# Performance work log

Measured on AMD Instinct MI355X. Metric: run time of the kernel, lower is better.

The kernel has to match this reference:

```python
import jax, jax.numpy as jnp
import numpy as np

DIM = 512
HEADS = 8
HEAD_DIM = DIM // HEADS
SCALE = HEAD_DIM ** -0.5


def setup_inputs() -> dict:
    key = jax.random.key(0)
    k1, k2, k3, k4, k5 = jax.random.split(key, 5)
    x = jax.random.normal(k1, (2, 4096, DIM), dtype=jnp.float32)
    # qkv Linear: weight [3*dim, dim], bias [3*dim]; proj: [dim, dim], [dim]
    w_qkv = jax.random.normal(k2, (3 * DIM, DIM), dtype=jnp.float32) * (DIM ** -0.5)
    b_qkv = jax.random.normal(k3, (3 * DIM,), dtype=jnp.float32) * 0.02
    w_proj = jax.random.normal(k4, (DIM, DIM), dtype=jnp.float32) * (DIM ** -0.5)
    b_proj = jax.random.normal(k5, (DIM,), dtype=jnp.float32) * 0.02
    return {"x": x, "w_qkv": w_qkv, "b_qkv": b_qkv, "w_proj": w_proj, "b_proj": b_proj}


def reference(x, w_qkv, b_qkv, w_proj, b_proj):
    B, N, C = x.shape
    qkv = x @ w_qkv.T + b_qkv  # [B, N, 3C]
    qkv = qkv.reshape(B, N, 3, HEADS, HEAD_DIM).transpose(2, 0, 3, 1, 4)  # [3,B,H,N,hd]
    q, k, v = qkv[0], qkv[1], qkv[2]
    attn = jnp.einsum('bhnd,bhmd->bhnm', q, k) * SCALE  # explicit NxN matrix
    attn = jax.nn.softmax(attn, axis=-1)
    out = jnp.einsum('bhnm,bhmd->bhnd', attn, v)  # [B,H,N,hd]
    out = out.transpose(0, 2, 1, 3).reshape(B, N, C)
    return out @ w_proj.T + b_proj
```

## Files before the change

### kernel.cpp

```cpp
#include <hip/hip_runtime.h>

typedef __bf16 bf16x8 __attribute__((ext_vector_type(8)));
typedef __bf16 bf16x4 __attribute__((ext_vector_type(4)));
typedef __bf16 bf16x2 __attribute__((ext_vector_type(2)));
typedef float  floatx4 __attribute__((ext_vector_type(4)));
typedef unsigned int uint32;
typedef uint32 uintx4 __attribute__((ext_vector_type(4)));

#define MFMA16(a,b,c) __builtin_amdgcn_mfma_f32_16x16x32_bf16(a,b,c,0,0,0)

constexpr int DIM  = 512;
constexpr int SEQ  = 4096;
constexpr int HD   = 64;
constexpr float QSCALE = 0.1803368801111244f;

static __device__ inline __bf16 f2bf(float f) {
    unsigned int u = __builtin_bit_cast(unsigned int, f);
    u += 0x7fffu + ((u >> 16) & 1u);
    return __builtin_bit_cast(__bf16, (unsigned short)(u >> 16));
}
#if __has_builtin(__builtin_amdgcn_cvt_pk_bf16_f32)
static __device__ inline bf16x2 pk2(float a, float b) {
    return __builtin_amdgcn_cvt_pk_bf16_f32(a, b);
}
#else
static __device__ inline bf16x2 pk2(float a, float b) {
    bf16x2 r; r[0] = f2bf(a); r[1] = f2bf(b); return r;
}
#endif
#if __has_builtin(__builtin_amdgcn_exp2f)
#define EXP2(x) __builtin_amdgcn_exp2f(x)
#else
#define EXP2(x) exp2f(x)
#endif
static __device__ inline bf16x8 cvt8(floatx4 lo, floatx4 hi) {
    uintx4 w;
    w[0] = __builtin_bit_cast(uint32, pk2(lo[0], lo[1]));
    w[1] = __builtin_bit_cast(uint32, pk2(lo[2], lo[3]));
    w[2] = __builtin_bit_cast(uint32, pk2(hi[0], hi[1]));
    w[3] = __builtin_bit_cast(uint32, pk2(hi[2], hi[3]));
    return __builtin_bit_cast(bf16x8, w);
}

static __device__ inline void gload16(const __bf16* g, __bf16* l) {
#if __has_builtin(__builtin_amdgcn_global_load_lds)
    __builtin_amdgcn_global_load_lds(
        (const __attribute__((address_space(1))) unsigned int*)g,
        (__attribute__((address_space(3))) unsigned int*)l, 16, 0, 0);
#else
    *(bf16x8*)(l + (threadIdx.x & 63)*8) = *(const bf16x8*)g;
#endif
}


__global__ __launch_bounds__(256)
void cvt_bf16(const float* __restrict__ X, const float* __restrict__ Wq,
              const float* __restrict__ Wp,
              __bf16* __restrict__ Xb, __bf16* __restrict__ Wqb,
              __bf16* __restrict__ Wpb)
{
    const int slice = blockIdx.y;
    const float* src;
    __bf16* dst;
    int n8;
    if (slice == 0)      { src = X;  dst = Xb;  n8 = (2*SEQ*DIM)/8; }
    else if (slice == 1) { src = Wq; dst = Wqb; n8 = (3*DIM*DIM)/8; }
    else                 { src = Wp; dst = Wpb; n8 = (DIM*DIM)/8; }
    const int i = blockIdx.x * 256 + threadIdx.x;
    if (i >= n8) return;
    const floatx4 lo = *(const floatx4*)(src + (size_t)i*8);
    const floatx4 hi = *(const floatx4*)(src + (size_t)i*8 + 4);
    *(bf16x8*)(dst + (size_t)i*8) = cvt8(lo, hi);
}

__global__ __launch_bounds__(256)
void gemm_qkv(const __bf16* __restrict__ X, const __bf16* __restrict__ W,
              const float* __restrict__ bias,
              __bf16* __restrict__ Qb, __bf16* __restrict__ Kb, __bf16* __restrict__ Vb)
{
    __shared__ __bf16 As[2][128*32];
    __shared__ __bf16 Bs[2][128*32];
    const int tid  = threadIdx.x;
    const int lane = tid & 63;
    const int wave = tid >> 6;
    const int quad = lane >> 4;
    const int l16  = lane & 15;
    const int waveM = wave >> 1, waveN = wave & 1;
    const int mBase = blockIdx.x * 128;
    const int nBase = blockIdx.y * 128;
    const int which = nBase >> 9;

    floatx4 zero = {0.f, 0.f, 0.f, 0.f};
    floatx4 acc[4][4];
    for (int i = 0; i < 4; i++)
        for (int j = 0; j < 4; j++) acc[i][j] = zero;

    const int lrow = lane >> 2;
    const int lcol = (lane & 3) * 8;

    const __bf16* ga = X + (size_t)(mBase + wave*16 + lrow)*DIM + lcol;
    const __bf16* gb = W + (size_t)(nBase + wave*16 + lrow)*DIM + lcol;

    auto STAGE = [&](int it, int b) {
        const int k0 = it * 32;
        gload16(ga + k0,            &As[b][(wave*16)*32]);
        gload16(ga + 64*DIM + k0,   &As[b][(64 + wave*16)*32]);
        gload16(gb + k0,            &Bs[b][(wave*16)*32]);
        gload16(gb + 64*DIM + k0,   &Bs[b][(64 + wave*16)*32]);
    };

    STAGE(0, 0);
    __syncthreads();

    for (int it = 0; it < 16; ++it) {
        const int cur = it & 1;
        if (it < 15) STAGE(it + 1, cur ^ 1);

        bf16x8 af[4], bfr[4];
        for (int mi = 0; mi < 4; mi++)
            af[mi]  = *(const bf16x8*)&As[cur][(waveM*64 + mi*16 + l16)*32 + quad*8];
        for (int ni = 0; ni < 4; ni++)
            bfr[ni] = *(const bf16x8*)&Bs[cur][(waveN*64 + ni*16 + l16)*32 + quad*8];
        if (which == 2) {
            for (int mi = 0; mi < 4; mi++)
                for (int ni = 0; ni < 4; ni++)
                    acc[mi][ni] = MFMA16(af[mi], bfr[ni], acc[mi][ni]);
        } else {
            for (int mi = 0; mi < 4; mi++)
                for (int ni = 0; ni < 4; ni++)
                    acc[mi][ni] = MFMA16(bfr[ni], af[mi], acc[mi][ni]);
        }
        __syncthreads();
    }

    if (which == 2) {
        for (int ni = 0; ni < 4; ni++) {
            const int n = nBase + waveN*64 + ni*16 + l16;
            const float bv = bias[n];
            const int h = (n >> 6) & 7;
            const int d = n & 63;
            for (int mi = 0; mi < 4; mi++) {
                const int m0 = mBase + waveM*64 + mi*16 + quad*4;
                const int b  = m0 >> 12;
                const int s0 = m0 & 4095;
                const int bh = (b << 3) | h;
                bf16x4 v;
                for (int rr = 0; rr < 4; rr++) v[rr] = f2bf(acc[mi][ni][rr] + bv);
                size_t off = (((((size_t)bh*128 + (s0 >> 5))*4 + (d >> 4))*64)
                              + ((s0 >> 2) & 3)*16 + (d & 15))*8 + ((s0 >> 4) & 1)*4;
                *(bf16x4*)&Vb[off] = v;
            }
        }
    } else {
        __bf16* dst = (which == 0) ? Qb : Kb;
        for (int ni = 0; ni < 4; ni++) {
            const int n0 = nBase + waveN*64 + ni*16 + quad*4;
            const floatx4 b4 = *(const floatx4*)&bias[n0];
            const int dfull = n0 & 511;
            const int h  = dfull >> 6;
            const int d0 = dfull & 63;
            const int lgrp = ((d0 >> 3) & 3)*16 + l16;
            const int half = d0 >> 5;
            const int slot = d0 & 7;
            for (int mi = 0; mi < 4; mi++) {
                const int m = mBase + waveM*64 + mi*16 + l16;
                const int b = m >> 12, s = m & 4095;
                const int bh = (b << 3) | h;
                bf16x4 v;
                for (int rr = 0; rr < 4; rr++) {
                    float val = acc[mi][ni][rr] + b4[rr];
                    if (which == 0) val *= QSCALE;
                    v[rr] = f2bf(val);
                }
                size_t off = ((((size_t)bh*256 + (s >> 4))*2 + half)*64 + lgrp)*8 + slot;
                *(bf16x4*)&dst[off] = v;
            }
        }
    }
}

__global__ __launch_bounds__(256, 3)
void attn_kernel(const __bf16* __restrict__ Qb, const __bf16* __restrict__ Kb,
                 const __bf16* __restrict__ Vb, __bf16* __restrict__ Ao)
{
    __shared__ __bf16 Ob[3][64*68];
    __shared__ float  Lb[4][64];
    const int tid  = threadIdx.x;
    const int lane = tid & 63;
    const int wave = tid >> 6;
    const int quad = lane >> 4;
    const int l16  = lane & 15;
    const int id    = blockIdx.x;
    const int slot  = id >> 3;
    const int bh    = (id & 7) + ((slot >> 6) << 3);
    const int qBase = (slot & 63) * 64;

    const __bf16* qg = Qb + (size_t)bh*256*2*512;
    const __bf16* kg = Kb + (size_t)bh*256*2*512;
    const __bf16* vg = Vb + (size_t)bh*128*4*512;

    bf16x8 qf[4][2];
    for (int t = 0; t < 4; t++)
        for (int hb = 0; hb < 2; hb++)
            qf[t][hb] = *(const bf16x8*)(qg
                + ((size_t)((qBase >> 4) + t)*2 + hb)*512 + lane*8);

    floatx4 zero = {0.f, 0.f, 0.f, 0.f};
    floatx4 oacc[4][4];
    for (int t = 0; t < 4; t++)
        for (int od = 0; od < 4; od++) oacc[t][od] = zero;
    floatx4 Lt[4];
    for (int t = 0; t < 4; t++) Lt[t] = zero;

    bf16x8 ones;
    for (int j = 0; j < 8; j++) ones[j] = f2bf(1.0f);

    const int key_begin = wave * 1024;
    const __bf16* kptr = kg + (size_t)(key_begin >> 4)*1024 + lane*8;
    const __bf16* vptr = vg + (size_t)(key_begin >> 5)*2048 + lane*8;

    for (int c = 0; c < 32; ++c) {
        bf16x8 kb00 = *(const bf16x8*)(kptr);
        bf16x8 kb01 = *(const bf16x8*)(kptr + 512);
        bf16x8 kb10 = *(const bf16x8*)(kptr + 1024);
        bf16x8 kb11 = *(const bf16x8*)(kptr + 1536);
        bf16x8 vb0  = *(const bf16x8*)(vptr);
        bf16x8 vb1  = *(const bf16x8*)(vptr + 512);
        bf16x8 vb2  = *(const bf16x8*)(vptr + 1024);
        bf16x8 vb3  = *(const bf16x8*)(vptr + 1536);
        kptr += 2048;
        vptr += 2048;

        for (int t = 0; t < 4; t++) {
            floatx4 z0 = zero, z1 = zero;
            z0 = MFMA16(kb00, qf[t][0], z0);
            z0 = MFMA16(kb01, qf[t][1], z0);
            z1 = MFMA16(kb10, qf[t][0], z1);
            z1 = MFMA16(kb11, qf[t][1], z1);
            float e0[4], e1[4];
            for (int r = 0; r < 4; r++) { e0[r] = EXP2(z0[r]); e1[r] = EXP2(z1[r]); }
            uintx4 w;
            w[0] = __builtin_bit_cast(uint32, pk2(e0[0], e0[1]));
            w[1] = __builtin_bit_cast(uint32, pk2(e0[2], e0[3]));
            w[2] = __builtin_bit_cast(uint32, pk2(e1[0], e1[1]));
            w[3] = __builtin_bit_cast(uint32, pk2(e1[2], e1[3]));
            bf16x8 pb = __builtin_bit_cast(bf16x8, w);
            Lt[t] = MFMA16(ones, pb, Lt[t]);
            oacc[t][0] = MFMA16(vb0, pb, oacc[t][0]);
            oacc[t][1] = MFMA16(vb1, pb, oacc[t][1]);
            oacc[t][2] = MFMA16(vb2, pb, oacc[t][2]);
            oacc[t][3] = MFMA16(vb3, pb, oacc[t][3]);
        }
    }

    if (lane < 16)
        for (int t = 0; t < 4; t++) Lb[wave][t*16 + lane] = Lt[t][0];
    __syncthreads();
    float inv[4];
    for (int t = 0; t < 4; t++) {
        const int q = t*16 + l16;
        inv[t] = 1.0f / (Lb[0][q] + Lb[1][q] + Lb[2][q] + Lb[3][q]);
    }
    if (wave != 0) {
        for (int t = 0; t < 4; t++)
            for (int od = 0; od < 4; od++) {
                bf16x4 v;
                for (int r = 0; r < 4; r++) v[r] = f2bf(oacc[t][od][r] * inv[t]);
                *(bf16x4*)&Ob[wave-1][(t*16 + l16)*68 + od*16 + quad*4] = v;
            }
    }
    __syncthreads();
    if (wave == 0) {
        const int b = bh >> 3, h = bh & 7;
        for (int t = 0; t < 4; t++) {
            const int s = qBase + t*16 + l16;
            for (int od = 0; od < 4; od++) {
                bf16x4 o0 = *(const bf16x4*)&Ob[0][(t*16 + l16)*68 + od*16 + quad*4];
                bf16x4 o1 = *(const bf16x4*)&Ob[1][(t*16 + l16)*68 + od*16 + quad*4];
                bf16x4 o2 = *(const bf16x4*)&Ob[2][(t*16 + l16)*68 + od*16 + quad*4];
                bf16x4 v;
                for (int r = 0; r < 4; r++) {
                    float o = oacc[t][od][r] * inv[t] +
                              (float)o0[r] + (float)o1[r] + (float)o2[r];
                    v[r] = f2bf(o);
                }
                *(bf16x4*)&Ao[((size_t)(b*SEQ + s))*DIM + h*HD + od*16 + quad*4] = v;
            }
        }
    }
}

__global__ __launch_bounds__(256)
void gemm_proj(const __bf16* __restrict__ A, const __bf16* __restrict__ W,
               const float* __restrict__ bias, float* __restrict__ Out)
{
    __shared__ __bf16 As[2][64*32];
    __shared__ __bf16 Bs[2][64*32];
    const int tid  = threadIdx.x;
    const int lane = tid & 63;
    const int wave = tid >> 6;
    const int quad = lane >> 4;
    const int l16  = lane & 15;
    const int waveM = wave >> 1, waveN = wave & 1;
    const int mBase = blockIdx.x * 64;
    const int nBase = blockIdx.y * 64;

    floatx4 zero = {0.f, 0.f, 0.f, 0.f};
    floatx4 acc[2][2];
    for (int i = 0; i < 2; i++)
        for (int j = 0; j < 2; j++) acc[i][j] = zero;

    const int lrow = lane >> 2;
    const int lcol = (lane & 3) * 8;

    const __bf16* gA = A + (size_t)(mBase + wave*16 + lrow)*DIM + lcol;
    const __bf16* gB = W + (size_t)(nBase + wave*16 + lrow)*DIM + lcol;

    auto STAGE = [&](int it, int b) {
        const int k0 = it * 32;
        gload16(gA + k0, &As[b][(wave*16)*32]);
        gload16(gB + k0, &Bs[b][(wave*16)*32]);
    };

    STAGE(0, 0);
    __syncthreads();

    for (int it = 0; it < 16; ++it) {
        const int cur = it & 1;
        if (it < 15) STAGE(it + 1, cur ^ 1);

        bf16x8 af[2], bfr[2];
        for (int mi = 0; mi < 2; mi++)
            af[mi]  = *(const bf16x8*)&As[cur][(waveM*32 + mi*16 + l16)*32 + quad*8];
        for (int ni = 0; ni < 2; ni++)
            bfr[ni] = *(const bf16x8*)&Bs[cur][(waveN*32 + ni*16 + l16)*32 + quad*8];
        for (int mi = 0; mi < 2; mi++)
            for (int ni = 0; ni < 2; ni++)
                acc[mi][ni] = MFMA16(af[mi], bfr[ni], acc[mi][ni]);
        __syncthreads();
    }

    for (int ni = 0; ni < 2; ni++) {
        const int n = nBase + waveN*32 + ni*16 + l16;
        const float bv = bias[n];
        for (int mi = 0; mi < 2; mi++) {
            const int m0 = mBase + waveM*32 + mi*16 + quad*4;
            for (int rr = 0; rr < 4; rr++)
                Out[(size_t)(m0 + rr)*DIM + n] = acc[mi][ni][rr] + bv;
        }
    }
}

extern "C" void kernel_launch(void* const* d_in, const int* in_sizes, int n_in,
                              void* d_out, int out_size, void* d_ws, size_t ws_size,
                              hipStream_t stream) {
    const float* x      = (const float*)d_in[0];
    const float* w_qkv  = (const float*)d_in[1];
    const float* b_qkv  = (const float*)d_in[2];
    const float* w_proj = (const float*)d_in[3];
    const float* b_proj = (const float*)d_in[4];
    float* out = (float*)d_out;

    __bf16* ws  = (__bf16*)d_ws;
    const size_t PLANE = (size_t)16 * SEQ * HD;
    __bf16* Qbk = ws;
    __bf16* Kbk = ws + PLANE;
    __bf16* Vbk = ws + 2*PLANE;
    __bf16* Aob = ws + 3*PLANE;
    __bf16* Xb  = ws + 4*PLANE;
    __bf16* Wqb = ws + 5*PLANE;
    __bf16* Wpb = ws + 5*PLANE + (size_t)3*DIM*DIM;

    cvt_bf16<<<dim3(2048, 3), 256, 0, stream>>>(x, w_qkv, w_proj, Xb, Wqb, Wpb);
    gemm_qkv<<<dim3(64, 12), 256, 0, stream>>>(Xb, Wqb, b_qkv, Qbk, Kbk, Vbk);
    attn_kernel<<<dim3(1024), 256, 0, stream>>>(Qbk, Kbk, Vbk, Aob);
    gemm_proj<<<dim3(128, 8), 256, 0, stream>>>(Aob, Wpb, b_proj, out);
}
```

Baseline: 194.6 us.

## Deepen QKV and projection GEMM pipelines to triple-buffered async loads

Both GEMM kernels move from double to triple LDS buffering and prefetch two K-steps ahead. Full __syncthreads is replaced by explicit vmcnt waits that leave the newest stage in flight, followed by a raw s_barrier. The goal is to hide global-load latency behind MFMA work. The cost is more LDS per block, which can lower occupancy, and it relies on hand-written waitcnt counts matching the number of gload16 calls per stage.

```diff
diff --git a/kernel.cpp b/kernel.cpp
--- a/kernel.cpp
+++ b/kernel.cpp
@@ -78,8 +78,8 @@
               const float* __restrict__ bias,
               __bf16* __restrict__ Qb, __bf16* __restrict__ Kb, __bf16* __restrict__ Vb)
 {
-    __shared__ __bf16 As[2][128*32];
-    __shared__ __bf16 Bs[2][128*32];
+    __shared__ __bf16 As[3][128*32];
+    __shared__ __bf16 Bs[3][128*32];
     const int tid  = threadIdx.x;
     const int lane = tid & 63;
     const int wave = tid >> 6;
@@ -110,11 +110,14 @@
     };
 
     STAGE(0, 0);
-    __syncthreads();
+    STAGE(1, 1);
+    asm volatile("s_waitcnt vmcnt(4)" ::: "memory");
+    __builtin_amdgcn_sched_barrier(0);
+    __builtin_amdgcn_s_barrier();
 
     for (int it = 0; it < 16; ++it) {
-        const int cur = it & 1;
-        if (it < 15) STAGE(it + 1, cur ^ 1);
+        const int cur = it % 3;
+        if (it < 14) STAGE(it + 2, (it + 2) % 3);
 
         bf16x8 af[4], bfr[4];
         for (int mi = 0; mi < 4; mi++)
@@ -130,7 +133,13 @@
                 for (int ni = 0; ni < 4; ni++)
                     acc[mi][ni] = MFMA16(bfr[ni], af[mi], acc[mi][ni]);
         }
-        __syncthreads();
+
+        if (it < 14)
+            asm volatile("s_waitcnt vmcnt(4) lgkmcnt(0)" ::: "memory");
+        else
+            asm volatile("s_waitcnt vmcnt(0) lgkmcnt(0)" ::: "memory");
+        __builtin_amdgcn_sched_barrier(0);
+        if (it < 15) __builtin_amdgcn_s_barrier();
     }
 
     if (which == 2) {
@@ -294,8 +303,8 @@
 void gemm_proj(const __bf16* __restrict__ A, const __bf16* __restrict__ W,
                const float* __restrict__ bias, float* __restrict__ Out)
 {
-    __shared__ __bf16 As[2][64*32];
-    __shared__ __bf16 Bs[2][64*32];
+    __shared__ __bf16 As[3][64*32];
+    __shared__ __bf16 Bs[3][64*32];
     const int tid  = threadIdx.x;
     const int lane = tid & 63;
     const int wave = tid >> 6;
@@ -323,11 +332,14 @@
     };
 
     STAGE(0, 0);
-    __syncthreads();
+    STAGE(1, 1);
+    asm volatile("s_waitcnt vmcnt(2)" ::: "memory");
+    __builtin_amdgcn_sched_barrier(0);
+    __builtin_amdgcn_s_barrier();
 
     for (int it = 0; it < 16; ++it) {
-        const int cur = it & 1;
-        if (it < 15) STAGE(it + 1, cur ^ 1);
+        const int cur = it % 3;
+        if (it < 14) STAGE(it + 2, (it + 2) % 3);
 
         bf16x8 af[2], bfr[2];
         for (int mi = 0; mi < 2; mi++)
@@ -337,7 +349,13 @@
         for (int mi = 0; mi < 2; mi++)
             for (int ni = 0; ni < 2; ni++)
                 acc[mi][ni] = MFMA16(af[mi], bfr[ni], acc[mi][ni]);
-        __syncthreads();
+
+        if (it < 14)
+            asm volatile("s_waitcnt vmcnt(2) lgkmcnt(0)" ::: "memory");
+        else
+            asm volatile("s_waitcnt vmcnt(0) lgkmcnt(0)" ::: "memory");
+        __builtin_amdgcn_sched_barrier(0);
+        if (it < 15) __builtin_amdgcn_s_barrier();
     }
 
     for (int ni = 0; ni < 2; ni++) {
```

New measurement: 192.7 us. About the same (-0.9%).

## Pre-block GEMM operands into MFMA fragment layout and load directly from global

Applied to the files above, without the earlier changes.

The conversion kernel and the attention output store now write X, the weights and the attention output in a blocked layout matching the 16x16x32 MFMA fragment order. The QKV and projection GEMMs then read fragments straight from global memory with contiguous 16-byte loads per lane, dropping LDS staging, double buffering and the per-iteration barriers. The cost is that tiles shared between waves are no longer reused through LDS, so more traffic goes through L2/L1, and loads are no longer prefetched ahead of the MFMAs.

```diff
diff --git a/kernel.cpp b/kernel.cpp
--- a/kernel.cpp
+++ b/kernel.cpp
@@ -42,22 +42,12 @@
     return __builtin_bit_cast(bf16x8, w);
 }
 
-static __device__ inline void gload16(const __bf16* g, __bf16* l) {
-#if __has_builtin(__builtin_amdgcn_global_load_lds)
-    __builtin_amdgcn_global_load_lds(
-        (const __attribute__((address_space(1))) unsigned int*)g,
-        (__attribute__((address_space(3))) unsigned int*)l, 16, 0, 0);
-#else
-    *(bf16x8*)(l + (threadIdx.x & 63)*8) = *(const bf16x8*)g;
-#endif
-}
-
 
 __global__ __launch_bounds__(256)
-void cvt_bf16(const float* __restrict__ X, const float* __restrict__ Wq,
-              const float* __restrict__ Wp,
-              __bf16* __restrict__ Xb, __bf16* __restrict__ Wqb,
-              __bf16* __restrict__ Wpb)
+void cvt_blk(const float* __restrict__ X, const float* __restrict__ Wq,
+             const float* __restrict__ Wp,
+             __bf16* __restrict__ Xb, __bf16* __restrict__ Wqb,
+             __bf16* __restrict__ Wpb)
 {
     const int slice = blockIdx.y;
     const float* src;
@@ -68,18 +58,20 @@
     else                 { src = Wp; dst = Wpb; n8 = (DIM*DIM)/8; }
     const int i = blockIdx.x * 256 + threadIdx.x;
     if (i >= n8) return;
+    const int row = i >> 6;
+    const int d0  = (i & 63) * 8;
     const floatx4 lo = *(const floatx4*)(src + (size_t)i*8);
     const floatx4 hi = *(const floatx4*)(src + (size_t)i*8 + 4);
-    *(bf16x8*)(dst + (size_t)i*8) = cvt8(lo, hi);
+    const size_t off8 = ((size_t)(row >> 4)*16 + (d0 >> 5))*64
+                        + ((d0 >> 3) & 3)*16 + (row & 15);
+    *(bf16x8*)(dst + off8*8) = cvt8(lo, hi);
 }
 
 __global__ __launch_bounds__(256)
-void gemm_qkv(const __bf16* __restrict__ X, const __bf16* __restrict__ W,
+void gemm_qkv(const __bf16* __restrict__ Xb, const __bf16* __restrict__ Wb,
               const float* __restrict__ bias,
               __bf16* __restrict__ Qb, __bf16* __restrict__ Kb, __bf16* __restrict__ Vb)
 {
-    __shared__ __bf16 As[2][128*32];
-    __shared__ __bf16 Bs[2][128*32];
     const int tid  = threadIdx.x;
     const int lane = tid & 63;
     const int wave = tid >> 6;
@@ -95,32 +87,15 @@
     for (int i = 0; i < 4; i++)
         for (int j = 0; j < 4; j++) acc[i][j] = zero;
 
-    const int lrow = lane >> 2;
-    const int lcol = (lane & 3) * 8;
-
-    const __bf16* ga = X + (size_t)(mBase + wave*16 + lrow)*DIM + lcol;
-    const __bf16* gb = W + (size_t)(nBase + wave*16 + lrow)*DIM + lcol;
-
-    auto STAGE = [&](int it, int b) {
-        const int k0 = it * 32;
-        gload16(ga + k0,            &As[b][(wave*16)*32]);
-        gload16(ga + 64*DIM + k0,   &As[b][(64 + wave*16)*32]);
-        gload16(gb + k0,            &Bs[b][(wave*16)*32]);
-        gload16(gb + 64*DIM + k0,   &Bs[b][(64 + wave*16)*32]);
-    };
-
-    STAGE(0, 0);
-    __syncthreads();
+    const __bf16* ga = Xb + (size_t)(mBase + waveM*64)*512 + lane*8;
+    const __bf16* gb = Wb + (size_t)(nBase + waveN*64)*512 + lane*8;
 
     for (int it = 0; it < 16; ++it) {
-        const int cur = it & 1;
-        if (it < 15) STAGE(it + 1, cur ^ 1);
-
         bf16x8 af[4], bfr[4];
         for (int mi = 0; mi < 4; mi++)
-            af[mi]  = *(const bf16x8*)&As[cur][(waveM*64 + mi*16 + l16)*32 + quad*8];
+            af[mi]  = *(const bf16x8*)(ga + mi*8192 + it*512);
         for (int ni = 0; ni < 4; ni++)
-            bfr[ni] = *(const bf16x8*)&Bs[cur][(waveN*64 + ni*16 + l16)*32 + quad*8];
+            bfr[ni] = *(const bf16x8*)(gb + ni*8192 + it*512);
         if (which == 2) {
             for (int mi = 0; mi < 4; mi++)
                 for (int ni = 0; ni < 4; ni++)
@@ -130,7 +105,6 @@
                 for (int ni = 0; ni < 4; ni++)
                     acc[mi][ni] = MFMA16(bfr[ni], af[mi], acc[mi][ni]);
         }
-        __syncthreads();
     }
 
     if (which == 2) {
@@ -273,7 +247,7 @@
     if (wave == 0) {
         const int b = bh >> 3, h = bh & 7;
         for (int t = 0; t < 4; t++) {
-            const int s = qBase + t*16 + l16;
+            const size_t rtop = (size_t)b*256 + (qBase >> 4) + t;
             for (int od = 0; od < 4; od++) {
                 bf16x4 o0 = *(const bf16x4*)&Ob[0][(t*16 + l16)*68 + od*16 + quad*4];
                 bf16x4 o1 = *(const bf16x4*)&Ob[1][(t*16 + l16)*68 + od*16 + quad*4];
@@ -284,18 +258,18 @@
                               (float)o0[r] + (float)o1[r] + (float)o2[r];
                     v[r] = f2bf(o);
                 }
-                *(bf16x4*)&Ao[((size_t)(b*SEQ + s))*DIM + h*HD + od*16 + quad*4] = v;
+                const size_t off8 = (rtop*16 + h*2 + (od >> 1))*64
+                                    + ((od*2 + (quad >> 1)) & 3)*16 + l16;
+                *(bf16x4*)&Ao[off8*8 + (quad & 1)*4] = v;
             }
         }
     }
 }
 
 __global__ __launch_bounds__(256)
-void gemm_proj(const __bf16* __restrict__ A, const __bf16* __restrict__ W,
+void gemm_proj(const __bf16* __restrict__ Ab, const __bf16* __restrict__ Wb,
                const float* __restrict__ bias, float* __restrict__ Out)
 {
-    __shared__ __bf16 As[2][64*32];
-    __shared__ __bf16 Bs[2][64*32];
     const int tid  = threadIdx.x;
     const int lane = tid & 63;
     const int wave = tid >> 6;
@@ -310,34 +284,18 @@
     for (int i = 0; i < 2; i++)
         for (int j = 0; j < 2; j++) acc[i][j] = zero;
 
-    const int lrow = lane >> 2;
-    const int lcol = (lane & 3) * 8;
-
-    const __bf16* gA = A + (size_t)(mBase + wave*16 + lrow)*DIM + lcol;
-    const __bf16* gB = W + (size_t)(nBase + wave*16 + lrow)*DIM + lcol;
-
-    auto STAGE = [&](int it, int b) {
-        const int k0 = it * 32;
-        gload16(gA + k0, &As[b][(wave*16)*32]);
-        gload16(gB + k0, &Bs[b][(wave*16)*32]);
-    };
-
-    STAGE(0, 0);
-    __syncthreads();
+    const __bf16* gA = Ab + (size_t)(mBase + waveM*32)*512 + lane*8;
+    const __bf16* gB = Wb + (size_t)(nBase + waveN*32)*512 + lane*8;
 
     for (int it = 0; it < 16; ++it) {
-        const int cur = it & 1;
-        if (it < 15) STAGE(it + 1, cur ^ 1);
-
         bf16x8 af[2], bfr[2];
         for (int mi = 0; mi < 2; mi++)
-            af[mi]  = *(const bf16x8*)&As[cur][(waveM*32 + mi*16 + l16)*32 + quad*8];
+            af[mi]  = *(const bf16x8*)(gA + mi*8192 + it*512);
         for (int ni = 0; ni < 2; ni++)
-            bfr[ni] = *(const bf16x8*)&Bs[cur][(waveN*32 + ni*16 + l16)*32 + quad*8];
+            bfr[ni] = *(const bf16x8*)(gB + ni*8192 + it*512);
         for (int mi = 0; mi < 2; mi++)
             for (int ni = 0; ni < 2; ni++)
                 acc[mi][ni] = MFMA16(af[mi], bfr[ni], acc[mi][ni]);
-        __syncthreads();
     }
 
     for (int ni = 0; ni < 2; ni++) {
@@ -371,7 +329,7 @@
     __bf16* Wqb = ws + 5*PLANE;
     __bf16* Wpb = ws + 5*PLANE + (size_t)3*DIM*DIM;
 
-    cvt_bf16<<<dim3(2048, 3), 256, 0, stream>>>(x, w_qkv, w_proj, Xb, Wqb, Wpb);
+    cvt_blk<<<dim3(2048, 3), 256, 0, stream>>>(x, w_qkv, w_proj, Xb, Wqb, Wpb);
     gemm_qkv<<<dim3(64, 12), 256, 0, stream>>>(Xb, Wqb, b_qkv, Qbk, Kbk, Vbk);
     attn_kernel<<<dim3(1024), 256, 0, stream>>>(Qbk, Kbk, Vbk, Aob);
     gemm_proj<<<dim3(128, 8), 256, 0, stream>>>(Aob, Wpb, b_proj, out);
```

Measured after the change: 184.1 us, median of 2. 1.06x faster.
